# Performance work log

Hardware: AMD Instinct MI355X
Metric: run time of the kernel (lower is better)

The kernel has to match this reference:

```python
import jax, jax.numpy as jnp
import numpy as np
from functools import partial

BN_EPS = 1e-5

def conv2d(x, w, pad):
    # x: [N,C,H,W], w: [O,I,kh,kw]
    return jax.lax.conv_general_dilated(
        x, w, window_strides=(1, 1), padding=((pad, pad), (pad, pad)),
        dimension_numbers=("NCHW", "OIHW", "NCHW"))

def bn_prelu(x, gamma, beta, mean, var, alpha):
    # eval-mode BatchNorm2d followed by single-parameter PReLU
    scale = gamma * jax.lax.rsqrt(var + BN_EPS)
    h = x * scale[None, :, None, None] + (beta - mean * scale)[None, :, None, None]
    return jnp.where(h >= 0, h, alpha * h)

def unfold3x3(x):
    # torch nn.Unfold(3, padding=1): output layout [N, C*9, H*W]
    N, C, H, W = x.shape
    xp = jnp.pad(x, ((0, 0), (0, 0), (1, 1), (1, 1)))
    patches = jnp.stack(
        [xp[:, :, i:i + H, j:j + W] for i in range(3) for j in range(3)],
        axis=2)  # [N, C, 9, H, W] -- row-major identical to [N, C*9, H*W]
    return patches

def setup_inputs() -> dict:
    key = jax.random.key(0)
    ks = jax.random.split(key, 16)
    N, C, H, W = 16, 256, 64, 64
    K2 = 9
    inp = {
        "x": jax.random.normal(ks[0], (N, C, H, W), jnp.float32),
        "y": jax.random.normal(ks[1], (N, C, H, W), jnp.float32),
        # gernerate_kernel_spatial[0]: Conv3x3 C->C + BN + PReLU
        "W1": jax.random.normal(ks[2], (C, C, 3, 3), jnp.float32) * 0.05,
        "g1": jax.random.normal(ks[3], (C,), jnp.float32) * 0.1 + 1.0,
        "b1": jax.random.normal(ks[4], (C,), jnp.float32) * 0.1,
        "m1": jax.random.normal(ks[5], (C,), jnp.float32) * 0.1,
        "v1": jax.random.uniform(ks[6], (C,), jnp.float32, 0.5, 1.5),
        "a1": jnp.float32(0.25),
        # gernerate_kernel_spatial[1]: Conv1x1 C->9 + BN + PReLU
        "W2": jax.random.normal(ks[7], (K2, C, 1, 1), jnp.float32) * 0.05,
        "g2": jax.random.normal(ks[8], (K2,), jnp.float32) * 0.1 + 1.0,
        "b2": jax.random.normal(ks[9], (K2,), jnp.float32) * 0.1,
        "m2": jax.random.normal(ks[10], (K2,), jnp.float32) * 0.1,
        "v2": jax.random.uniform(ks[11], (K2,), jnp.float32, 0.5, 1.5),
        "a2": jnp.float32(0.25),
    }
    return inp

def reference(x, y, W1, g1, b1, m1, v1, a1, W2, g2, b2, m2, v2, a2):
    N, C, H, W = x.shape
    # dynamic per-pixel 3x3 kernel from y: [N, 9, H, W]
    h = bn_prelu(conv2d(y, W1, pad=1), g1, b1, m1, v1, a1)
    kernel = bn_prelu(conv2d(h, W2, pad=0), g2, b2, m2, v2, a2)
    # kernel.reshape(N,9,H,W,1).permute(0,2,3,1,4) -> [N,H,W,9]
    kern = jnp.transpose(kernel, (0, 2, 3, 1))
    # unfold(x) is [N, C*9, H*W]; torch reshapes it ROW-MAJOR to [N,H,W,C,9]
    ux = unfold3x3(x).reshape(N, H, W, C, 9)
    # matmul [N,H,W,C,9] @ [N,H,W,9,1] -> squeeze -> permute to NCHW
    out = jnp.einsum("nhwck,nhwk->nchw", ux, kern)
    return out
```

## Files before the change

kernel.cpp:

```cpp
#include <hip/hip_runtime.h>
#include <hip/hip_bf16.h>

typedef __attribute__((ext_vector_type(8))) short bf16x8;
typedef __attribute__((ext_vector_type(4))) float f32x4;
typedef __attribute__((ext_vector_type(8))) unsigned short u16x8;
typedef __attribute__((ext_vector_type(4))) unsigned short u16x4;

#define BN_EPS 1e-5f

__device__ __forceinline__ unsigned short f2bf(float f) {
  unsigned int u = __float_as_uint(f);
  unsigned int r = u + 0x7FFFu + ((u >> 16) & 1u);
  return (unsigned short)(r >> 16);
}
__device__ __forceinline__ float bf2f(unsigned short u) {
  union { float f; unsigned int i; } v; v.i = ((unsigned int)u) << 16; return v.f;
}

__device__ __forceinline__ void async_ld16(const unsigned short* g, unsigned short* l) {
  __builtin_amdgcn_global_load_lds(
      (const __attribute__((address_space(1))) void*)g,
      (__attribute__((address_space(3))) void*)l, 16, 0, 0);
}

__global__ __launch_bounds__(256) void params_kernel(
    const float* __restrict__ g1, const float* __restrict__ b1,
    const float* __restrict__ m1, const float* __restrict__ v1,
    const float* __restrict__ W2, const float* __restrict__ g2,
    const float* __restrict__ b2, const float* __restrict__ m2,
    const float* __restrict__ v2,
    float* __restrict__ bias1, float* __restrict__ W2f, float* __restrict__ bias2)
{
  int t = threadIdx.x;
  {
    float s = g1[t] * rsqrtf(v1[t] + BN_EPS);
    bias1[t] = b1[t] - m1[t] * s;
  }
  for (int i = t; i < 2304; i += 256) {
    int j = i >> 8;
    float s2 = g2[j] * rsqrtf(v2[j] + BN_EPS);
    W2f[i] = W2[i] * s2;
  }
  if (t < 9) {
    float s2 = g2[t] * rsqrtf(v2[t] + BN_EPS);
    bias2[t] = b2[t] - m2[t] * s2;
  }
}

__global__ __launch_bounds__(256) void fold_w1_kernel(
    const float* __restrict__ W1, const float* __restrict__ g1,
    const float* __restrict__ v1, unsigned short* __restrict__ Bt)
{
  int o = blockIdx.x;
  int t = threadIdx.x;
  float s = g1[o] * rsqrtf(v1[o] + BN_EPS);
  const float* src = W1 + (size_t)o * 2304 + (size_t)t * 9;
  int chunk = t >> 5, q = (t >> 3) & 3, e = t & 7;
  #pragma unroll
  for (int tap = 0; tap < 9; ++tap) {
    float wv = src[tap] * s;
    Bt[((((size_t)tap * 8 + chunk) * 4 + q) * 256 + o) * 8 + e] = f2bf(wv);
  }
}

__global__ __launch_bounds__(256) void border_zero_kernel(unsigned short* __restrict__ yTp)
{
  int p = blockIdx.x;
  int t = threadIdx.x;
  size_t base = (size_t)p * (66 * 66 * 8);
  u16x8 z = (u16x8){0, 0, 0, 0, 0, 0, 0, 0};
  if (t < 66) {
    *(u16x8*)(yTp + base + (size_t)t * 8) = z;
    *(u16x8*)(yTp + base + ((size_t)65 * 66 + t) * 8) = z;
  }
  if (t >= 128 && t < 192) {
    int hh = t - 127;
    *(u16x8*)(yTp + base + ((size_t)hh * 66) * 8) = z;
    *(u16x8*)(yTp + base + ((size_t)hh * 66 + 65) * 8) = z;
  }
}

__global__ __launch_bounds__(256) void transpose_pad_kernel(
    const float* __restrict__ y, unsigned short* __restrict__ yTp)
{
  __shared__ unsigned short T[64][68];
  int t = threadIdx.x;
  int nb = blockIdx.x; int n = nb >> 6, h = nb & 63;
  int w4 = (t & 15) * 4;
  int cl = t >> 4;
  for (int cb = 0; cb < 4; ++cb) {
    __syncthreads();
    #pragma unroll
    for (int r = 0; r < 4; ++r) {
      int c = cb * 64 + cl + r * 16;
      float4 v = *(const float4*)(y + ((((size_t)n * 256 + c) * 64 + h) << 6) + w4);
      u16x4 pv = { f2bf(v.x), f2bf(v.y), f2bf(v.z), f2bf(v.w) };
      *(u16x4*)&T[cl + r * 16][w4] = pv;
    }
    __syncthreads();
    size_t base = ((((size_t)n * 32 + cb * 8) * 66 + (h + 1)) * 66 + 1) * 8;
    #pragma unroll
    for (int pass = 0; pass < 2; ++pass) {
      int w = pass * 32 + (t >> 3);
      int c8 = t & 7;
      u16x8 o;
      #pragma unroll
      for (int i = 0; i < 8; ++i) o[i] = T[c8 * 8 + i][w];
      *(u16x8*)(yTp + base + ((size_t)c8 * (66 * 66) + w) * 8) = o;
    }
  }
}

__global__ __launch_bounds__(256, 2) void conv3x3_mfma_kernel(
    const unsigned short* __restrict__ yTp, const unsigned short* __restrict__ Bt,
    const float* __restrict__ bias1, const float* __restrict__ a1p,
    unsigned short* __restrict__ hT)
{
  __shared__ unsigned short Als[2][4][4][66][8];
  __shared__ unsigned short Bls[2][4][256][8];
  int tid = threadIdx.x;
  int w = tid >> 6, l = tid & 63;
  int lr = l & 15, quad = l >> 4;
  int wm = w >> 1, wn = w & 1;
  int bm = blockIdx.x;
  int n = bm >> 5, hb = (bm & 31) * 2;

  f32x4 acc[4][8];
  #pragma unroll
  for (int im = 0; im < 4; ++im)
    #pragma unroll
    for (int in_ = 0; in_ < 8; ++in_)
      acc[im][in_] = (f32x4){0.f, 0.f, 0.f, 0.f};

  const unsigned short* gaBase = yTp + (size_t)n * 32 * (66 * 66 * 8);

  auto stageA = [&](int chunk, int buf) {
    int qg0 = chunk * 4;
    #pragma unroll
    for (int q = 0; q < 4; ++q) {
      const unsigned short* ga = gaBase +
          (((size_t)(qg0 + q) * 66 + (hb + w)) * 66 + l) * 8;
      async_ld16(ga, &Als[buf][q][w][0][0]);
    }
    if (l < 2) {
      #pragma unroll
      for (int q = 0; q < 4; ++q) {
        const unsigned short* ga = gaBase +
            (((size_t)(qg0 + q) * 66 + (hb + w)) * 66 + 64 + l) * 8;
        async_ld16(ga, &Als[buf][q][w][64][0]);
      }
    }
  };
  auto stageB = [&](int tap, int chunk, int buf) {
    #pragma unroll
    for (int q = 0; q < 4; ++q) {
      const unsigned short* gb = Bt +
          ((((size_t)tap * 8 + chunk) * 4 + q) * 256 + w * 64 + l) * 8;
      async_ld16(gb, &Bls[buf][q][w * 64][0]);
    }
  };

  stageA(0, 0);
  stageB(0, 0, 0);

  int ab = 0, bb = 0;
  #pragma unroll 1
  for (int c = 0; c < 8; ++c) {
    #pragma unroll 1
    for (int t = 0; t < 9; ++t) {
      __syncthreads();
      if (t < 8) stageB(t + 1, c, bb ^ 1);
      else if (c < 7) stageB(0, c + 1, bb ^ 1);
      if (t == 0 && c < 7) stageA(c + 1, ab ^ 1);

      int ti = t / 3, tj = t - 3 * ti;
      bf16x8 af[4], bfr[8];
      #pragma unroll
      for (int im = 0; im < 4; ++im)
        af[im] = *(const bf16x8*)&Als[ab][quad][wm + ti][im * 16 + lr + tj][0];
      #pragma unroll
      for (int in_ = 0; in_ < 8; ++in_)
        bfr[in_] = *(const bf16x8*)&Bls[bb][quad][wn * 128 + in_ * 16 + lr][0];
      #pragma unroll
      for (int im = 0; im < 4; ++im)
        #pragma unroll
        for (int in_ = 0; in_ < 8; ++in_)
          acc[im][in_] = __builtin_amdgcn_mfma_f32_16x16x32_bf16(
              af[im], bfr[in_], acc[im][in_], 0, 0, 0);

      bb ^= 1;
    }
    ab ^= 1;
  }

  float a1 = a1p[0];
  size_t pix0 = (size_t)bm * 128 + wm * 64;
  #pragma unroll
  for (int in_ = 0; in_ < 8; ++in_) {
    int c = wn * 128 + in_ * 16 + lr;
    float bs = bias1[c];
    #pragma unroll
    for (int im = 0; im < 4; ++im) {
      size_t m0 = pix0 + im * 16 + quad * 4;
      #pragma unroll
      for (int r = 0; r < 4; ++r) {
        float v = acc[im][in_][r] + bs;
        v = (v >= 0.f) ? v : a1 * v;
        hT[(m0 + r) * 256 + c] = f2bf(v);
      }
    }
  }
}

__global__ __launch_bounds__(256) void conv1x1_kernel(
    const unsigned short* __restrict__ hT, const float* __restrict__ W2f,
    const float* __restrict__ bias2, const float* __restrict__ a2p,
    float* __restrict__ kernP)
{
  __shared__ float w2s[2304];
  int t = threadIdx.x;
  for (int i = t; i < 2304; i += 256) w2s[i] = W2f[i];
  __syncthreads();
  int seg = t & 3;
  int pr = t >> 2;
  int p = blockIdx.x * 64 + pr;
  const unsigned short* hp = hT + (size_t)p * 256;
  float acc[9];
  #pragma unroll
  for (int j = 0; j < 9; ++j) acc[j] = 0.f;
  for (int c0 = seg * 8; c0 < 256; c0 += 32) {
    u16x8 hv = *(const u16x8*)(hp + c0);
    float hf[8];
    #pragma unroll
    for (int i = 0; i < 8; ++i) hf[i] = bf2f(hv[i]);
    #pragma unroll
    for (int j = 0; j < 9; ++j)
      #pragma unroll
      for (int i = 0; i < 8; ++i)
        acc[j] = fmaf(hf[i], w2s[j * 256 + c0 + i], acc[j]);
  }
  #pragma unroll
  for (int j = 0; j < 9; ++j) {
    acc[j] += __shfl_xor(acc[j], 1);
    acc[j] += __shfl_xor(acc[j], 2);
  }
  if (seg == 0) {
    float a2 = a2p[0];
    #pragma unroll
    for (int j = 0; j < 9; ++j) {
      float v = acc[j] + bias2[j];
      v = (v >= 0.f) ? v : a2 * v;
      kernP[j * 65536 + p] = v;
    }
  }
}

__global__ __launch_bounds__(256) void apply_dyn_kernel(
    const float* __restrict__ x, const float* __restrict__ kernP,
    float* __restrict__ out)
{
  __shared__ float xs[66 * 67];
  __shared__ float ks[9][16];
  int t = threadIdx.x;
  int b = blockIdx.x;
  int g = b & 3;
  int nh = b >> 2;
  int n = nh >> 6, hp = nh & 63;
  int c = 4 * hp + g;

  const float* xplane = x + (((size_t)n * 256 + c) << 12);
  for (int i = t; i < 1024; i += 256) {
    float4 v = *(const float4*)(xplane + i * 4);
    int row = i >> 4;
    int col = (i & 15) * 4;
    float* d = &xs[(row + 1) * 67 + col + 1];
    d[0] = v.x; d[1] = v.y; d[2] = v.z; d[3] = v.w;
  }
  if (t < 67) { xs[t] = 0.f; xs[65 * 67 + t] = 0.f; }
  if (t < 128) { int r = (t >> 1) + 1; int cc = (t & 1) * 65; xs[r * 67 + cc] = 0.f; }
  int pbase = n * 4096 + hp * 64 + g * 16;
  for (int i = t; i < 144; i += 256)
    ks[i / 16][i & 15] = kernP[(i / 16) * 65536 + pbase + (i & 15)];
  __syncthreads();

  int s = t & 15;
  int crow = t >> 4;
  float ksr[9];
  #pragma unroll
  for (int k2 = 0; k2 < 9; ++k2) ksr[k2] = ks[k2][s];

  int r0 = s * 2304 + crow * 144;
  int k0 = r0 >> 12;
  int rem0 = r0 & 4095;
  int wcol = rem0 & 63;
  int ti0 = (k0 >= 6) ? 2 : ((k0 >= 3) ? 1 : 0);
  int tj0 = k0 - 3 * ti0;
  int addr = (rem0 >> 6) * 67 + wcol + ti0 * 67 + tj0;
  int cnt = 4096 - rem0;
  int kN = k0 + 1;
  int tiN = (kN >= 6) ? 2 : ((kN >= 3) ? 1 : 0);
  int addrAtCross = tiN * 67 + (kN - 3 * tiN);

  size_t outIdx = (((size_t)n * 256 + crow * 16) << 12) + (hp << 6) + g * 16 + s;
  #pragma unroll 4
  for (int oi = 0; oi < 16; ++oi) {
    float acc = 0.f;
    #pragma unroll
    for (int k2 = 0; k2 < 9; ++k2) {
      acc = fmaf(xs[addr], ksr[k2], acc);
      ++wcol; ++addr;
      if (wcol == 64) { wcol = 0; addr += 3; }
      if (--cnt == 0) addr = addrAtCross;
    }
    out[outIdx + ((size_t)oi << 12)] = acc;
  }
}

extern "C" void kernel_launch(void* const* d_in, const int* in_sizes, int n_in,
                              void* d_out, int out_size, void* d_ws, size_t ws_size,
                              hipStream_t stream) {
  const float* x  = (const float*)d_in[0];
  const float* y  = (const float*)d_in[1];
  const float* W1 = (const float*)d_in[2];
  const float* g1 = (const float*)d_in[3];
  const float* b1 = (const float*)d_in[4];
  const float* m1 = (const float*)d_in[5];
  const float* v1 = (const float*)d_in[6];
  const float* a1 = (const float*)d_in[7];
  const float* W2 = (const float*)d_in[8];
  const float* g2 = (const float*)d_in[9];
  const float* b2 = (const float*)d_in[10];
  const float* m2 = (const float*)d_in[11];
  const float* v2 = (const float*)d_in[12];
  const float* a2 = (const float*)d_in[13];
  float* out = (float*)d_out;

  char* ws = (char*)d_ws;
  size_t off = 0;
  const size_t yTp_bytes = (size_t)16 * 66 * 66 * 256 * 2;
  unsigned short* yTp = (unsigned short*)(ws + off); off += yTp_bytes;
  unsigned short* Bt  = (unsigned short*)(ws + off); off += (size_t)589824 * 2;
  unsigned short* hT  = (unsigned short*)(ws + off); off += (size_t)16777216 * 2;
  float* kernP = (float*)(ws + off); off += (size_t)589824 * 4;
  float* bias1 = (float*)(ws + off); off += 1024;
  float* W2f   = (float*)(ws + off); off += 9216;
  float* bias2 = (float*)(ws + off); off += 64;

  params_kernel<<<1, 256, 0, stream>>>(g1, b1, m1, v1, W2, g2, b2, m2, v2,
                                       bias1, W2f, bias2);
  fold_w1_kernel<<<256, 256, 0, stream>>>(W1, g1, v1, Bt);
  border_zero_kernel<<<512, 256, 0, stream>>>(yTp);
  transpose_pad_kernel<<<1024, 256, 0, stream>>>(y, yTp);
  conv3x3_mfma_kernel<<<512, 256, 0, stream>>>(yTp, Bt, bias1, a1, hT);
  conv1x1_kernel<<<1024, 256, 0, stream>>>(hT, W2f, bias2, a2, kernP);
  apply_dyn_kernel<<<4096, 256, 0, stream>>>(x, kernP, out);
}
```

Measured before the change: 324.5 us.

## Fuse conv1x1 epilogue into conv3x3 MFMA kernel and merge setup kernels

The 1x1 conv, BN and PReLU are now computed inside the conv3x3 kernel's epilogue. The bf16 activation tile is staged in shared memory that reuses the A/B buffers through a union, so the 32MB hT intermediate never goes to global memory. The params kernel is folded into fold_w1, and border zeroing is folded into the transpose kernel, which removes two launches. The main loop is also unrolled over pairs of channel chunks with constant buffer indices and s_setprio around the MFMAs. The added shared memory for w2s and the union, plus the larger epilogue, may lower occupancy or raise register pressure.

```diff
diff --git a/kernel.cpp b/kernel.cpp
--- a/kernel.cpp
+++ b/kernel.cpp
@@ -23,36 +23,30 @@
       (__attribute__((address_space(3))) void*)l, 16, 0, 0);
 }
 
-__global__ __launch_bounds__(256) void params_kernel(
-    const float* __restrict__ g1, const float* __restrict__ b1,
-    const float* __restrict__ m1, const float* __restrict__ v1,
-    const float* __restrict__ W2, const float* __restrict__ g2,
-    const float* __restrict__ b2, const float* __restrict__ m2,
-    const float* __restrict__ v2,
-    float* __restrict__ bias1, float* __restrict__ W2f, float* __restrict__ bias2)
-{
-  int t = threadIdx.x;
-  {
-    float s = g1[t] * rsqrtf(v1[t] + BN_EPS);
-    bias1[t] = b1[t] - m1[t] * s;
-  }
-  for (int i = t; i < 2304; i += 256) {
-    int j = i >> 8;
-    float s2 = g2[j] * rsqrtf(v2[j] + BN_EPS);
-    W2f[i] = W2[i] * s2;
-  }
-  if (t < 9) {
-    float s2 = g2[t] * rsqrtf(v2[t] + BN_EPS);
-    bias2[t] = b2[t] - m2[t] * s2;
-  }
-}
-
 __global__ __launch_bounds__(256) void fold_w1_kernel(
     const float* __restrict__ W1, const float* __restrict__ g1,
-    const float* __restrict__ v1, unsigned short* __restrict__ Bt)
+    const float* __restrict__ b1, const float* __restrict__ m1,
+    const float* __restrict__ v1, const float* __restrict__ W2,
+    const float* __restrict__ g2, const float* __restrict__ b2,
+    const float* __restrict__ m2, const float* __restrict__ v2,
+    unsigned short* __restrict__ Bt, float* __restrict__ bias1,
+    float* __restrict__ W2f, float* __restrict__ bias2)
 {
   int o = blockIdx.x;
   int t = threadIdx.x;
+  if (o == 0) {
+    float s1 = g1[t] * rsqrtf(v1[t] + BN_EPS);
+    bias1[t] = b1[t] - m1[t] * s1;
+    for (int i = t; i < 2304; i += 256) {
+      int j = i >> 8;
+      float s2 = g2[j] * rsqrtf(v2[j] + BN_EPS);
+      W2f[i] = W2[i] * s2;
+    }
+    if (t < 9) {
+      float s2 = g2[t] * rsqrtf(v2[t] + BN_EPS);
+      bias2[t] = b2[t] - m2[t] * s2;
+    }
+  }
   float s = g1[o] * rsqrtf(v1[o] + BN_EPS);
   const float* src = W1 + (size_t)o * 2304 + (size_t)t * 9;
   int chunk = t >> 5, q = (t >> 3) & 3, e = t & 7;
@@ -60,23 +54,6 @@
   for (int tap = 0; tap < 9; ++tap) {
     float wv = src[tap] * s;
     Bt[((((size_t)tap * 8 + chunk) * 4 + q) * 256 + o) * 8 + e] = f2bf(wv);
-  }
-}
-
-__global__ __launch_bounds__(256) void border_zero_kernel(unsigned short* __restrict__ yTp)
-{
-  int p = blockIdx.x;
-  int t = threadIdx.x;
-  size_t base = (size_t)p * (66 * 66 * 8);
-  u16x8 z = (u16x8){0, 0, 0, 0, 0, 0, 0, 0};
-  if (t < 66) {
-    *(u16x8*)(yTp + base + (size_t)t * 8) = z;
-    *(u16x8*)(yTp + base + ((size_t)65 * 66 + t) * 8) = z;
-  }
-  if (t >= 128 && t < 192) {
-    int hh = t - 127;
-    *(u16x8*)(yTp + base + ((size_t)hh * 66) * 8) = z;
-    *(u16x8*)(yTp + base + ((size_t)hh * 66 + 65) * 8) = z;
   }
 }
 
@@ -109,15 +86,34 @@
       *(u16x8*)(yTp + base + ((size_t)c8 * (66 * 66) + w) * 8) = o;
     }
   }
+  u16x8 z = (u16x8){0, 0, 0, 0, 0, 0, 0, 0};
+  size_t nb32 = (size_t)n * 32;
+  if (t < 64) {
+    int qg = t & 31, side = t >> 5;
+    *(u16x8*)(yTp + (((nb32 + qg) * 66 + (h + 1)) * 66 + side * 65) * 8) = z;
+  }
+  if (h == 0) {
+    for (int i = t; i < 2112; i += 256) {
+      int qg = i / 66, ww = i - qg * 66;
+      *(u16x8*)(yTp + (((nb32 + qg) * 66 + 0) * 66 + ww) * 8) = z;
+      *(u16x8*)(yTp + (((nb32 + qg) * 66 + 65) * 66 + ww) * 8) = z;
+    }
+  }
 }
 
 __global__ __launch_bounds__(256, 2) void conv3x3_mfma_kernel(
     const unsigned short* __restrict__ yTp, const unsigned short* __restrict__ Bt,
     const float* __restrict__ bias1, const float* __restrict__ a1p,
-    unsigned short* __restrict__ hT)
+    const float* __restrict__ W2f, const float* __restrict__ bias2,
+    const float* __restrict__ a2p, float* __restrict__ kernP)
 {
-  __shared__ unsigned short Als[2][4][4][66][8];
-  __shared__ unsigned short Bls[2][4][256][8];
+  __shared__ union SM {
+    struct { unsigned short A[2][4][4][66][8];
+             unsigned short B[2][4][256][8]; } m;
+    unsigned short h[128][264];
+  } sm;
+  __shared__ float w2s[2304];
+
   int tid = threadIdx.x;
   int w = tid >> 6, l = tid & 63;
   int lr = l & 15, quad = l >> 4;
@@ -125,6 +121,8 @@
   int bm = blockIdx.x;
   int n = bm >> 5, hb = (bm & 31) * 2;
 
+  for (int i = tid; i < 2304; i += 256) w2s[i] = W2f[i];
+
   f32x4 acc[4][8];
   #pragma unroll
   for (int im = 0; im < 4; ++im)
@@ -133,124 +131,120 @@
       acc[im][in_] = (f32x4){0.f, 0.f, 0.f, 0.f};
 
   const unsigned short* gaBase = yTp + (size_t)n * 32 * (66 * 66 * 8);
+  const unsigned short* gaW  = gaBase + ((size_t)(hb + w) * 66 + l) * 8;
+  const unsigned short* gaW2 = gaBase + ((size_t)(hb + w) * 66 + 64 + l) * 8;
+  const unsigned short* gbW  = Bt + (size_t)(w * 64 + l) * 8;
 
   auto stageA = [&](int chunk, int buf) {
-    int qg0 = chunk * 4;
-    #pragma unroll
-    for (int q = 0; q < 4; ++q) {
-      const unsigned short* ga = gaBase +
-          (((size_t)(qg0 + q) * 66 + (hb + w)) * 66 + l) * 8;
-      async_ld16(ga, &Als[buf][q][w][0][0]);
-    }
+    #pragma unroll
+    for (int q = 0; q < 4; ++q)
+      async_ld16(gaW + (size_t)(chunk * 4 + q) * (66 * 66 * 8),
+                 &sm.m.A[buf][q][w][0][0]);
     if (l < 2) {
       #pragma unroll
-      for (int q = 0; q < 4; ++q) {
-        const unsigned short* ga = gaBase +
-            (((size_t)(qg0 + q) * 66 + (hb + w)) * 66 + 64 + l) * 8;
-        async_ld16(ga, &Als[buf][q][w][64][0]);
-      }
+      for (int q = 0; q < 4; ++q)
+        async_ld16(gaW2 + (size_t)(chunk * 4 + q) * (66 * 66 * 8),
+                   &sm.m.A[buf][q][w][64][0]);
     }
   };
   auto stageB = [&](int tap, int chunk, int buf) {
-    #pragma unroll
-    for (int q = 0; q < 4; ++q) {
-      const unsigned short* gb = Bt +
-          ((((size_t)tap * 8 + chunk) * 4 + q) * 256 + w * 64 + l) * 8;
-      async_ld16(gb, &Bls[buf][q][w * 64][0]);
-    }
+    const unsigned short* gb = gbW + (size_t)tap * 65536 + (size_t)chunk * 8192;
+    #pragma unroll
+    for (int q = 0; q < 4; ++q)
+      async_ld16(gb + q * 2048, &sm.m.B[buf][q][w * 64][0]);
   };
 
   stageA(0, 0);
   stageB(0, 0, 0);
 
-  int ab = 0, bb = 0;
-  #pragma unroll 1
-  for (int c = 0; c < 8; ++c) {
-    #pragma unroll 1
-    for (int t = 0; t < 9; ++t) {
-      __syncthreads();
-      if (t < 8) stageB(t + 1, c, bb ^ 1);
-      else if (c < 7) stageB(0, c + 1, bb ^ 1);
-      if (t == 0 && c < 7) stageA(c + 1, ab ^ 1);
-
-      int ti = t / 3, tj = t - 3 * ti;
-      bf16x8 af[4], bfr[8];
-      #pragma unroll
-      for (int im = 0; im < 4; ++im)
-        af[im] = *(const bf16x8*)&Als[ab][quad][wm + ti][im * 16 + lr + tj][0];
-      #pragma unroll
-      for (int in_ = 0; in_ < 8; ++in_)
-        bfr[in_] = *(const bf16x8*)&Bls[bb][quad][wn * 128 + in_ * 16 + lr][0];
-      #pragma unroll
-      for (int im = 0; im < 4; ++im)
+  for (int cc = 0; cc < 8; cc += 2) {
+    #pragma unroll
+    for (int u = 0; u < 2; ++u) {
+      #pragma unroll
+      for (int t = 0; t < 9; ++t) {
+        __syncthreads();
+        int c = cc + u;
+        if (t < 8) stageB(t + 1, c, (u + t + 1) & 1);
+        else if (c < 7) stageB(0, c + 1, (u + t + 1) & 1);
+        if (t == 0 && c < 7) stageA(c + 1, u ^ 1);
+
+        const int ti = t / 3, tj = t % 3;
+        bf16x8 af[4], bfr[8];
+        #pragma unroll
+        for (int im = 0; im < 4; ++im)
+          af[im] = *(const bf16x8*)&sm.m.A[u][quad][wm + ti][im * 16 + lr + tj][0];
         #pragma unroll
         for (int in_ = 0; in_ < 8; ++in_)
-          acc[im][in_] = __builtin_amdgcn_mfma_f32_16x16x32_bf16(
-              af[im], bfr[in_], acc[im][in_], 0, 0, 0);
-
-      bb ^= 1;
-    }
-    ab ^= 1;
-  }
+          bfr[in_] = *(const bf16x8*)&sm.m.B[(u + t) & 1][quad][wn * 128 + in_ * 16 + lr][0];
+        __builtin_amdgcn_s_setprio(1);
+        #pragma unroll
+        for (int im = 0; im < 4; ++im)
+          #pragma unroll
+          for (int in_ = 0; in_ < 8; ++in_)
+            acc[im][in_] = __builtin_amdgcn_mfma_f32_16x16x32_bf16(
+                af[im], bfr[in_], acc[im][in_], 0, 0, 0);
+        __builtin_amdgcn_s_setprio(0);
+      }
+    }
+  }
+
+  __syncthreads();
 
   float a1 = a1p[0];
-  size_t pix0 = (size_t)bm * 128 + wm * 64;
   #pragma unroll
   for (int in_ = 0; in_ < 8; ++in_) {
-    int c = wn * 128 + in_ * 16 + lr;
-    float bs = bias1[c];
+    int cch = wn * 128 + in_ * 16 + lr;
+    float bs = bias1[cch];
     #pragma unroll
     for (int im = 0; im < 4; ++im) {
-      size_t m0 = pix0 + im * 16 + quad * 4;
+      int p0 = wm * 64 + im * 16 + quad * 4;
       #pragma unroll
       for (int r = 0; r < 4; ++r) {
         float v = acc[im][in_][r] + bs;
         v = (v >= 0.f) ? v : a1 * v;
-        hT[(m0 + r) * 256 + c] = f2bf(v);
+        sm.h[p0 + r][cch] = f2bf(v);
       }
     }
   }
-}
-
-__global__ __launch_bounds__(256) void conv1x1_kernel(
-    const unsigned short* __restrict__ hT, const float* __restrict__ W2f,
-    const float* __restrict__ bias2, const float* __restrict__ a2p,
-    float* __restrict__ kernP)
-{
-  __shared__ float w2s[2304];
-  int t = threadIdx.x;
-  for (int i = t; i < 2304; i += 256) w2s[i] = W2f[i];
   __syncthreads();
-  int seg = t & 3;
-  int pr = t >> 2;
-  int p = blockIdx.x * 64 + pr;
-  const unsigned short* hp = hT + (size_t)p * 256;
-  float acc[9];
-  #pragma unroll
-  for (int j = 0; j < 9; ++j) acc[j] = 0.f;
-  for (int c0 = seg * 8; c0 < 256; c0 += 32) {
-    u16x8 hv = *(const u16x8*)(hp + c0);
-    float hf[8];
-    #pragma unroll
-    for (int i = 0; i < 8; ++i) hf[i] = bf2f(hv[i]);
-    #pragma unroll
-    for (int j = 0; j < 9; ++j)
-      #pragma unroll
-      for (int i = 0; i < 8; ++i)
-        acc[j] = fmaf(hf[i], w2s[j * 256 + c0 + i], acc[j]);
-  }
-  #pragma unroll
-  for (int j = 0; j < 9; ++j) {
-    acc[j] += __shfl_xor(acc[j], 1);
-    acc[j] += __shfl_xor(acc[j], 2);
-  }
-  if (seg == 0) {
-    float a2 = a2p[0];
+
+  float a2 = a2p[0];
+  int seg = tid & 3, pr = tid >> 2;
+  float b2r[9];
+  #pragma unroll
+  for (int j = 0; j < 9; ++j) b2r[j] = bias2[j];
+  #pragma unroll
+  for (int rd = 0; rd < 2; ++rd) {
+    int pl = rd * 64 + pr;
+    float acc2[9];
+    #pragma unroll
+    for (int j = 0; j < 9; ++j) acc2[j] = 0.f;
+    #pragma unroll
+    for (int k = 0; k < 8; ++k) {
+      int c0 = seg * 8 + k * 32;
+      u16x8 hv = *(const u16x8*)&sm.h[pl][c0];
+      float hf[8];
+      #pragma unroll
+      for (int i = 0; i < 8; ++i) hf[i] = bf2f(hv[i]);
+      #pragma unroll
+      for (int j = 0; j < 9; ++j)
+        #pragma unroll
+        for (int i = 0; i < 8; ++i)
+          acc2[j] = fmaf(hf[i], w2s[j * 256 + c0 + i], acc2[j]);
+    }
     #pragma unroll
     for (int j = 0; j < 9; ++j) {
-      float v = acc[j] + bias2[j];
-      v = (v >= 0.f) ? v : a2 * v;
-      kernP[j * 65536 + p] = v;
+      acc2[j] += __shfl_xor(acc2[j], 1);
+      acc2[j] += __shfl_xor(acc2[j], 2);
+    }
+    if (seg == 0) {
+      size_t gp = (size_t)bm * 128 + pl;
+      #pragma unroll
+      for (int j = 0; j < 9; ++j) {
+        float v = acc2[j] + b2r[j];
+        v = (v >= 0.f) ? v : a2 * v;
+        kernP[j * 65536 + gp] = v;
+      }
     }
   }
 }
@@ -340,18 +334,15 @@
   const size_t yTp_bytes = (size_t)16 * 66 * 66 * 256 * 2;
   unsigned short* yTp = (unsigned short*)(ws + off); off += yTp_bytes;
   unsigned short* Bt  = (unsigned short*)(ws + off); off += (size_t)589824 * 2;
-  unsigned short* hT  = (unsigned short*)(ws + off); off += (size_t)16777216 * 2;
   float* kernP = (float*)(ws + off); off += (size_t)589824 * 4;
   float* bias1 = (float*)(ws + off); off += 1024;
   float* W2f   = (float*)(ws + off); off += 9216;
   float* bias2 = (float*)(ws + off); off += 64;
 
-  params_kernel<<<1, 256, 0, stream>>>(g1, b1, m1, v1, W2, g2, b2, m2, v2,
-                                       bias1, W2f, bias2);
-  fold_w1_kernel<<<256, 256, 0, stream>>>(W1, g1, v1, Bt);
-  border_zero_kernel<<<512, 256, 0, stream>>>(yTp);
+  fold_w1_kernel<<<256, 256, 0, stream>>>(W1, g1, b1, m1, v1, W2, g2, b2, m2, v2,
+                                          Bt, bias1, W2f, bias2);
   transpose_pad_kernel<<<1024, 256, 0, stream>>>(y, yTp);
-  conv3x3_mfma_kernel<<<512, 256, 0, stream>>>(yTp, Bt, bias1, a1, hT);
-  conv1x1_kernel<<<1024, 256, 0, stream>>>(hT, W2f, bias2, a2, kernP);
+  conv3x3_mfma_kernel<<<512, 256, 0, stream>>>(yTp, Bt, bias1, a1,
+                                               W2f, bias2, a2, kernP);
   apply_dyn_kernel<<<4096, 256, 0, stream>>>(x, kernP, out);
 }
```

Result: faster. 310.4 us (-4.3%).
